# Performance work log

Hardware: AMD Instinct MI355X
Metric: run time of the kernel (lower is better)

## Reference

```python
import jax, jax.numpy as jnp
import numpy as np

N, D, E, H, K = 8192, 1024, 8, 256, 2


def setup_inputs() -> dict:
    key = jax.random.key(0)
    ks = jax.random.split(key, 9)
    s = 0.02
    return {
        "x": jax.random.normal(ks[0], (N, D), dtype=jnp.float32),
        "Wg": jax.random.normal(ks[1], (D, E), dtype=jnp.float32) * s,
        "bg": jnp.zeros((E,), dtype=jnp.float32),
        "W1": jax.random.normal(ks[2], (E, D, H), dtype=jnp.float32) * s,
        "b1": jnp.zeros((E, H), dtype=jnp.float32),
        "W2": jax.random.normal(ks[3], (E, H, H), dtype=jnp.float32) * s,
        "b2": jnp.zeros((E, H), dtype=jnp.float32),
        "W3": jax.random.normal(ks[4], (E, H, D), dtype=jnp.float32) * s,
        "b3": jnp.zeros((E, D), dtype=jnp.float32),
    }


def reference(x, Wg, bg, W1, b1, W2, b2, W3, b3):
    # Gating: softmax over experts, then keep only top-k gate values per token.
    gates = jax.nn.softmax(x @ Wg + bg, axis=-1)              # [N, E]
    top_v, top_i = jax.lax.top_k(gates, K)                    # [N, K]
    rows = jnp.arange(gates.shape[0])[:, None]                # [N, 1]
    top_k_gates = jnp.zeros_like(gates).at[rows, top_i].set(top_v)  # [N, E]

    # Dense all-expert MLP (matches original: every expert runs on every token).
    h = jax.nn.relu(jnp.einsum('nd,edh->neh', x, W1) + b1)    # [N, E, H]
    h = jax.nn.relu(jnp.einsum('neh,ehg->neg', h, W2) + b2)   # [N, E, H]  (dropout is eval no-op)
    eo = jax.nn.relu(jnp.einsum('neh,ehd->ned', h, W3) + b3)  # [N, E, D]

    # Combine with masked gates: einsum('...nde,...ne->...nd') with eo in 'ned' layout.
    output = jnp.einsum('ned,ne->nd', eo, top_k_gates)        # [N, D]
    return output
```

## Files before the change

### kernel.cpp

```cpp
#include <hip/hip_runtime.h>
#include <math.h>

#define NTOK 8192
#define DDIM 1024
#define NEXP 8
#define HDIM 256
#define TOPK 2
#define PADM 128
#define CAPS (NTOK * TOPK + NEXP * PADM)
#define NT64  (CAPS / 64)

typedef __attribute__((ext_vector_type(8))) __bf16 bf16x8;
typedef __attribute__((ext_vector_type(4))) float f32x4;

#define GLDS16(g, s)                                                      \
    __builtin_amdgcn_global_load_lds(                                     \
        (const __attribute__((address_space(1))) void*)(g),               \
        (__attribute__((address_space(3))) void*)(s), 16, 0, 0)

static constexpr size_t OFF_TOFF = 128;
static constexpr size_t OFF_ZBUF = 4096;
static constexpr size_t OFF_T2E  = 8192;
static constexpr size_t OFF_T2G  = OFF_T2E + (size_t)NTOK * TOPK * 4;
static constexpr size_t OFF_SLOT = OFF_T2G + (size_t)NTOK * TOPK * 4;
static constexpr size_t OFF_TOK  = OFF_SLOT + (size_t)NTOK * TOPK * 4;
static constexpr size_t OFF_GAT  = OFF_TOK + (size_t)CAPS * 4;
static constexpr size_t OFF_XB   = (OFF_GAT + (size_t)CAPS * 4 + 255) & ~(size_t)255;
static constexpr size_t OFF_W1T  = OFF_XB  + (size_t)NTOK * DDIM * 2;
static constexpr size_t OFF_W2T  = OFF_W1T + (size_t)NEXP * DDIM * HDIM * 2;
static constexpr size_t OFF_W3T  = OFF_W2T + (size_t)NEXP * HDIM * HDIM * 2;
static constexpr size_t OFF_H2   = OFF_W3T + (size_t)NEXP * HDIM * DDIM * 2;
static constexpr size_t OFF_H3   = OFF_H2  + (size_t)CAPS * HDIM * 2;

static __device__ __forceinline__ unsigned short f2b(float f) {
    __bf16 h = (__bf16)f;
    return __builtin_bit_cast(unsigned short, h);
}
static __device__ __forceinline__ float b2f(unsigned short u) {
    return __builtin_bit_cast(float, ((unsigned)u) << 16);
}

__global__ __launch_bounds__(256) void gate_trans(
    const float* __restrict__ x, const float* __restrict__ Wg,
    const float* __restrict__ bg, unsigned short* __restrict__ xb,
    int* __restrict__ top2e, float* __restrict__ top2g,
    const float* __restrict__ W1, const float* __restrict__ W2,
    const float* __restrict__ W3, __bf16* __restrict__ w1t,
    __bf16* __restrict__ w2t, __bf16* __restrict__ w3t)
{
    __shared__ __align__(16) float sh[NEXP * DDIM];
    const int tid = threadIdx.x;

    if (blockIdx.x < 256) {
        for (int d = tid; d < DDIM; d += 256) {
            const float4 w0 = *(const float4*)(Wg + (size_t)d * NEXP);
            const float4 w1 = *(const float4*)(Wg + (size_t)d * NEXP + 4);
            sh[0 * DDIM + d] = w0.x; sh[1 * DDIM + d] = w0.y;
            sh[2 * DDIM + d] = w0.z; sh[3 * DDIM + d] = w0.w;
            sh[4 * DDIM + d] = w1.x; sh[5 * DDIM + d] = w1.y;
            sh[6 * DDIM + d] = w1.z; sh[7 * DDIM + d] = w1.w;
        }
        __syncthreads();

        const int n = (blockIdx.y * 256 + blockIdx.x) * 4 + (tid >> 6);
        const int lane = tid & 63;
        const float* xr = x + (size_t)n * DDIM;
        unsigned short* xbr = xb + (size_t)n * DDIM;

        float acc[NEXP];
#pragma unroll
        for (int e = 0; e < NEXP; ++e) acc[e] = 0.f;

#pragma unroll
        for (int it = 0; it < 4; ++it) {
            const int d = it * 256 + lane * 4;
            const float4 xv = *(const float4*)(xr + d);
            ushort4 u;
            u.x = f2b(xv.x); u.y = f2b(xv.y); u.z = f2b(xv.z); u.w = f2b(xv.w);
            *(ushort4*)(xbr + d) = u;
#pragma unroll
            for (int e = 0; e < NEXP; ++e) {
                const float4 wt = *(const float4*)(sh + e * DDIM + d);
                acc[e] = fmaf(xv.x, wt.x, acc[e]);
                acc[e] = fmaf(xv.y, wt.y, acc[e]);
                acc[e] = fmaf(xv.z, wt.z, acc[e]);
                acc[e] = fmaf(xv.w, wt.w, acc[e]);
            }
        }
#pragma unroll
        for (int off = 32; off > 0; off >>= 1)
#pragma unroll
            for (int e = 0; e < NEXP; ++e) acc[e] += __shfl_down(acc[e], off, 64);

        if (lane == 0) {
            float v[NEXP], mx = -1e30f;
#pragma unroll
            for (int e = 0; e < NEXP; ++e) { v[e] = acc[e] + bg[e]; mx = fmaxf(mx, v[e]); }
            float p[NEXP], s = 0.f;
#pragma unroll
            for (int e = 0; e < NEXP; ++e) { p[e] = expf(v[e] - mx); s += p[e]; }
            const float inv = 1.f / s;
#pragma unroll
            for (int e = 0; e < NEXP; ++e) p[e] *= inv;
            int i0 = 0;
#pragma unroll
            for (int e = 1; e < NEXP; ++e) if (p[e] > p[i0]) i0 = e;
            int i1 = (i0 == 0) ? 1 : 0;
#pragma unroll
            for (int e = 0; e < NEXP; ++e) if (e != i0 && p[e] > p[i1]) i1 = e;
            top2e[n * 2 + 0] = i0;  top2e[n * 2 + 1] = i1;
            top2g[n * 2 + 0] = p[i0]; top2g[n * 2 + 1] = p[i1];
        }
    } else {
        const int e = blockIdx.y;
        int bt = blockIdx.x - 256;
        const float* Wi; __bf16* Wo; int R, C, xt, yt;
        if (bt < 256)      { Wi = W1; Wo = w1t; R = DDIM; C = HDIM; xt = bt & 7;  yt = bt >> 3; }
        else if (bt < 320) { bt -= 256; Wi = W2; Wo = w2t; R = HDIM; C = HDIM; xt = bt & 7;  yt = bt >> 3; }
        else               { bt -= 320; Wi = W3; Wo = w3t; R = HDIM; C = DDIM; xt = bt & 31; yt = bt >> 5; }
        const int r0 = yt * 32, c0 = xt * 32;
        const int tx = tid & 31, ty = tid >> 5;
        const float* Wie = Wi + (size_t)e * R * C;
        __bf16* Woe = Wo + (size_t)e * C * R;
#pragma unroll
        for (int j = 0; j < 4; ++j)
            sh[(ty + j * 8) * 33 + tx] = Wie[(size_t)(r0 + ty + j * 8) * C + c0 + tx];
        __syncthreads();
#pragma unroll
        for (int j = 0; j < 4; ++j)
            Woe[(size_t)(c0 + ty + j * 8) * R + r0 + tx] = (__bf16)sh[tx * 33 + ty + j * 8];
    }
}

__global__ __launch_bounds__(1024) void route(
    const int* __restrict__ top2e, const float* __restrict__ top2g,
    int* __restrict__ toff, int* __restrict__ tok, float* __restrict__ gat,
    int* __restrict__ slotof, float* __restrict__ zbuf)
{
    const int tid = threadIdx.x;
    const int wv = tid >> 6, ln = tid & 63;
    __shared__ int   waveTot[16][NEXP];
    __shared__ int   waveBase[16][NEXP];
    __shared__ int   totS[NEXP];
    __shared__ int   toffS[NEXP + 1];
    __shared__ short excS[1024][NEXP];

    zbuf[tid] = 0.f;

    int myE[16]; float myG[16];
    const int4*   pe = (const int4*)(top2e + tid * 16);
    const float4* pg = (const float4*)(top2g + tid * 16);
#pragma unroll
    for (int q = 0; q < 4; ++q) {
        const int4 v = pe[q];
        myE[q * 4 + 0] = v.x; myE[q * 4 + 1] = v.y;
        myE[q * 4 + 2] = v.z; myE[q * 4 + 3] = v.w;
        const float4 g = pg[q];
        myG[q * 4 + 0] = g.x; myG[q * 4 + 1] = g.y;
        myG[q * 4 + 2] = g.z; myG[q * 4 + 3] = g.w;
    }

#pragma unroll
    for (int e = 0; e < NEXP; ++e) {
        int c = 0;
#pragma unroll
        for (int j = 0; j < 16; ++j) c += (myE[j] == e);
        int inc = c;
#pragma unroll
        for (int off = 1; off < 64; off <<= 1) {
            const int t = __shfl_up(inc, off, 64);
            if (ln >= off) inc += t;
        }
        excS[tid][e] = (short)(inc - c);
        if (ln == 63) waveTot[wv][e] = inc;
    }
    __syncthreads();

    if (tid < NEXP) {
        int b = 0;
#pragma unroll
        for (int w = 0; w < 16; ++w) {
            const int t = waveTot[w][tid];
            waveBase[w][tid] = b;
            b += t;
        }
        totS[tid] = b;
    }
    __syncthreads();

    if (tid == 0) {
        int acc = 0;
#pragma unroll
        for (int e = 0; e < NEXP; ++e) {
            toffS[e] = acc;
            acc += (totS[e] + PADM - 1) & ~(PADM - 1);
        }
        toffS[NEXP] = acc;
#pragma unroll
        for (int e = 0; e <= NEXP; ++e) toff[e] = toffS[e];
    }
    __syncthreads();

#pragma unroll
    for (int j = 0; j < 16; ++j) {
        int pre = 0;
#pragma unroll
        for (int j2 = 0; j2 < j; ++j2) pre += (myE[j2] == myE[j]);
        const int e = myE[j];
        const int slot = toffS[e] + waveBase[wv][e] + (int)excS[tid][e] + pre;
        const int i = tid * 16 + j;
        tok[slot] = i >> 1;
        gat[slot] = myG[j];
        slotof[i] = slot;
    }

#pragma unroll
    for (int e = 0; e < NEXP; ++e) {
        const int begin = toffS[e] + totS[e];
        const int end   = toffS[e + 1];
        for (int i = begin + tid; i < end; i += 1024) {
            tok[i] = -1;
            gat[i] = 0.f;
        }
    }
}

__global__ __launch_bounds__(256) void egemm123(
    const __bf16* __restrict__ xb, const __bf16* __restrict__ w1t,
    const __bf16* __restrict__ w2t, const __bf16* __restrict__ w3t,
    const float* __restrict__ b1, const float* __restrict__ b2,
    const float* __restrict__ b3, const int* __restrict__ toff,
    const int* __restrict__ tok, const float* __restrict__ gat,
    const char* __restrict__ zbuf, __bf16* __restrict__ h3)
{
    const int total = toff[NEXP];
    const int slot0 = blockIdx.x * 64;
    if (slot0 >= total) return;
    int e = 0;
    while (toff[e + 1] <= slot0) ++e;

    __shared__ __align__(16) char smem[73728];
    char* AsB = smem;
    char* BsB = smem + 8192;
    char* H1s = smem + 40960;

    const int tid  = threadIdx.x;
    const int lane = tid & 63;
    const int wid  = tid >> 6;

    const int srow  = tid >> 3;
    const int sslot = tid & 7;
    const int ks    = sslot ^ (srow & 7);

    const __bf16* We1 = w1t + (size_t)e * HDIM * DDIM;
    const char* ap[2];
#pragma unroll
    for (int i = 0; i < 2; ++i) {
        const int t = tok[slot0 + i * 32 + srow];
        ap[i] = (t >= 0) ? (const char*)(xb + (size_t)t * DDIM + ks * 8)
                         : (const char*)zbuf;
    }
    const char* bp1[8];
#pragma unroll
    for (int i = 0; i < 8; ++i)
        bp1[i] = (const char*)(We1 + (size_t)(i * 32 + srow) * DDIM + ks * 8);

    const int llo = lane & 15, lhi = lane >> 4;
    const int m7 = llo & 7;
    int abyte[4], bbyte[4];
#pragma unroll
    for (int m = 0; m < 4; ++m) {
        abyte[m] = (m * 16 + llo) * 128;
        bbyte[m] = (wid * 64 + m * 16 + llo) * 128;
    }

    f32x4 acc[4][4];
#pragma unroll
    for (int m = 0; m < 4; ++m)
#pragma unroll
        for (int n = 0; n < 4; ++n) acc[m][n] = (f32x4){0.f, 0.f, 0.f, 0.f};

    for (int k0 = 0; k0 < DDIM; k0 += 64) {
        const size_t kb = (size_t)k0 * 2;
        GLDS16(ap[0] + kb, AsB + tid * 16);
        GLDS16(ap[1] + kb, AsB + 4096 + tid * 16);
#pragma unroll
        for (int i = 0; i < 8; ++i)
            GLDS16(bp1[i] + kb, BsB + i * 4096 + tid * 16);
        __syncthreads();
#pragma unroll
        for (int kk = 0; kk < 2; ++kk) {
            const int sl = ((kk << 2) + lhi) ^ m7;
            bf16x8 af[4], bfr[4];
#pragma unroll
            for (int m = 0; m < 4; ++m) af[m]  = *(const bf16x8*)(AsB + abyte[m] + (sl << 4));
#pragma unroll
            for (int n = 0; n < 4; ++n) bfr[n] = *(const bf16x8*)(BsB + bbyte[n] + (sl << 4));
#pragma unroll
            for (int m = 0; m < 4; ++m)
#pragma unroll
                for (int n = 0; n < 4; ++n)
                    acc[m][n] = __builtin_amdgcn_mfma_f32_16x16x32_bf16(
                        af[m], bfr[n], acc[m][n], 0, 0, 0);
        }
        __syncthreads();
    }

    {
        const float* be1 = b1 + (size_t)e * HDIM;
#pragma unroll
        for (int n = 0; n < 4; ++n) {
            const int col = wid * 64 + n * 16 + llo;
            const float bb = be1[col];
            const int colbyte = (col & 7) * 2;
            const int slice = col >> 3;
#pragma unroll
            for (int m = 0; m < 4; ++m) {
#pragma unroll
                for (int j = 0; j < 4; ++j) {
                    const int r = m * 16 + lhi * 4 + j;
                    const float v = fmaxf(acc[m][n][j] + bb, 0.f);
                    *(__bf16*)(H1s + r * 512 + ((slice ^ (r & 7)) << 4) + colbyte) = (__bf16)v;
                }
                acc[m][n] = (f32x4){0.f, 0.f, 0.f, 0.f};
            }
        }
    }
    __syncthreads();

    const __bf16* We2 = w2t + (size_t)e * HDIM * HDIM;
    const char* bp2[8];
#pragma unroll
    for (int i = 0; i < 8; ++i)
        bp2[i] = (const char*)(We2 + (size_t)(i * 32 + srow) * HDIM + ks * 8);

    for (int k2 = 0; k2 < 4; ++k2) {
        const size_t kb = (size_t)k2 * 128;
#pragma unroll
        for (int i = 0; i < 8; ++i)
            GLDS16(bp2[i] + kb, BsB + i * 4096 + tid * 16);
        __syncthreads();
#pragma unroll
        for (int kk = 0; kk < 2; ++kk) {
            const int slB = ((kk << 2) + lhi) ^ m7;
            const int sA  = k2 * 8 + (kk << 2) + lhi;
            const int slA = sA ^ m7;
            bf16x8 af[4], bfr[4];
#pragma unroll
            for (int m = 0; m < 4; ++m)
                af[m] = *(const bf16x8*)(H1s + (m * 16 + llo) * 512 + (slA << 4));
#pragma unroll
            for (int n = 0; n < 4; ++n)
                bfr[n] = *(const bf16x8*)(BsB + bbyte[n] + (slB << 4));
#pragma unroll
            for (int m = 0; m < 4; ++m)
#pragma unroll
                for (int n = 0; n < 4; ++n)
                    acc[m][n] = __builtin_amdgcn_mfma_f32_16x16x32_bf16(
                        af[m], bfr[n], acc[m][n], 0, 0, 0);
        }
        __syncthreads();
    }

    {
        const float* be2 = b2 + (size_t)e * HDIM;
#pragma unroll
        for (int n = 0; n < 4; ++n) {
            const int col = wid * 64 + n * 16 + llo;
            const float bb = be2[col];
            const int colbyte = (col & 7) * 2;
            const int slice = col >> 3;
#pragma unroll
            for (int m = 0; m < 4; ++m) {
#pragma unroll
                for (int j = 0; j < 4; ++j) {
                    const int r = m * 16 + lhi * 4 + j;
                    const float v = fmaxf(acc[m][n][j] + bb, 0.f);
                    *(__bf16*)(H1s + r * 512 + ((slice ^ (r & 7)) << 4) + colbyte) = (__bf16)v;
                }
            }
        }
    }
    __syncthreads();

    const __bf16* We3 = w3t + (size_t)e * DDIM * HDIM;
    const float* be3 = b3 + (size_t)e * DDIM;
    float gv[4][4];
#pragma unroll
    for (int m = 0; m < 4; ++m)
#pragma unroll
        for (int j = 0; j < 4; ++j)
            gv[m][j] = gat[slot0 + m * 16 + lhi * 4 + j];

    for (int cc = 0; cc < 4; ++cc) {
#pragma unroll
        for (int m = 0; m < 4; ++m)
#pragma unroll
            for (int n = 0; n < 4; ++n) acc[m][n] = (f32x4){0.f, 0.f, 0.f, 0.f};

        for (int k2 = 0; k2 < 4; ++k2) {
            const size_t kb = (size_t)k2 * 128;
#pragma unroll
            for (int i = 0; i < 8; ++i)
                GLDS16((const char*)(We3 + (size_t)(cc * 256 + i * 32 + srow) * HDIM + ks * 8) + kb,
                       BsB + i * 4096 + tid * 16);
            __syncthreads();
#pragma unroll
            for (int kk = 0; kk < 2; ++kk) {
                const int slB = ((kk << 2) + lhi) ^ m7;
                const int sA  = k2 * 8 + (kk << 2) + lhi;
                const int slA = sA ^ m7;
                bf16x8 af[4], bfr[4];
#pragma unroll
                for (int m = 0; m < 4; ++m)
                    af[m] = *(const bf16x8*)(H1s + (m * 16 + llo) * 512 + (slA << 4));
#pragma unroll
                for (int n = 0; n < 4; ++n)
                    bfr[n] = *(const bf16x8*)(BsB + bbyte[n] + (slB << 4));
#pragma unroll
                for (int m = 0; m < 4; ++m)
#pragma unroll
                    for (int n = 0; n < 4; ++n)
                        acc[m][n] = __builtin_amdgcn_mfma_f32_16x16x32_bf16(
                            af[m], bfr[n], acc[m][n], 0, 0, 0);
            }
            __syncthreads();
        }

#pragma unroll
        for (int m = 0; m < 4; ++m) {
            const int rbase = slot0 + m * 16 + lhi * 4;
#pragma unroll
            for (int n = 0; n < 4; ++n) {
                const int col = cc * 256 + wid * 64 + n * 16 + llo;
                const float bb = be3[col];
#pragma unroll
                for (int j = 0; j < 4; ++j) {
                    const float v = fmaxf(acc[m][n][j] + bb, 0.f) * gv[m][j];
                    h3[(size_t)(rbase + j) * DDIM + col] = (__bf16)v;
                }
            }
        }
    }
}

__global__ __launch_bounds__(256) void combine(
    const unsigned short* __restrict__ h3, const int* __restrict__ slotof,
    float* __restrict__ out)
{
    const int n = blockIdx.x;
    const int c = threadIdx.x * 4;
    const int s0 = slotof[n * 2], s1 = slotof[n * 2 + 1];
    const ushort4 a = *(const ushort4*)(h3 + (size_t)s0 * DDIM + c);
    const ushort4 b = *(const ushort4*)(h3 + (size_t)s1 * DDIM + c);
    float4 o;
    o.x = b2f(a.x) + b2f(b.x);
    o.y = b2f(a.y) + b2f(b.y);
    o.z = b2f(a.z) + b2f(b.z);
    o.w = b2f(a.w) + b2f(b.w);
    *(float4*)(out + (size_t)n * DDIM + c) = o;
}

extern "C" void kernel_launch(void* const* d_in, const int* in_sizes, int n_in,
                              void* d_out, int out_size, void* d_ws, size_t ws_size,
                              hipStream_t stream)
{
    const float* x  = (const float*)d_in[0];
    const float* Wg = (const float*)d_in[1];
    const float* bg = (const float*)d_in[2];
    const float* W1 = (const float*)d_in[3];
    const float* b1 = (const float*)d_in[4];
    const float* W2 = (const float*)d_in[5];
    const float* b2 = (const float*)d_in[6];
    const float* W3 = (const float*)d_in[7];
    const float* b3 = (const float*)d_in[8];
    float* out = (float*)d_out;

    char* ws = (char*)d_ws;
    int*   toff   = (int*)(ws + OFF_TOFF);
    char*  zbuf   = ws + OFF_ZBUF;
    int*   top2e  = (int*)(ws + OFF_T2E);
    float* top2g  = (float*)(ws + OFF_T2G);
    int*   slotof = (int*)(ws + OFF_SLOT);
    int*   tok    = (int*)(ws + OFF_TOK);
    float* gat    = (float*)(ws + OFF_GAT);
    unsigned short* xbu = (unsigned short*)(ws + OFF_XB);
    __bf16* xb  = (__bf16*)(ws + OFF_XB);
    __bf16* w1t = (__bf16*)(ws + OFF_W1T);
    __bf16* w2t = (__bf16*)(ws + OFF_W2T);
    __bf16* w3t = (__bf16*)(ws + OFF_W3T);
    __bf16* h3  = (__bf16*)(ws + OFF_H3);

    gate_trans<<<dim3(832, NEXP), 256, 0, stream>>>(
        x, Wg, bg, xbu, top2e, top2g, W1, W2, W3, w1t, w2t, w3t);
    route<<<1, 1024, 0, stream>>>(top2e, top2g, toff, tok, gat, slotof, (float*)zbuf);

    egemm123<<<NT64, 256, 0, stream>>>(xb, w1t, w2t, w3t, b1, b2, b3,
                                       toff, tok, gat, zbuf, h3);

    combine<<<NTOK, 256, 0, stream>>>((const unsigned short*)h3, slotof, out);
}
```

Before: 112.0 us.

## Double-buffer LDS tiles across all three expert GEMM stages with cross-stage prefetch

Enlarges shared memory to hold two A/B tile buffers and prefetches the next k-tile with global_load_lds while MFMAs consume the current one. The prefetch also crosses stage boundaries: the first W2 tile is loaded during the last W1 step, and the first W3 tile during the last W2 step. The four W3 column chunks are flattened into one 16-step pipelined loop. The aim is to hide global load latency that the single-buffer load, sync, compute scheme exposed, at the cost of more LDS per block and a possible drop in occupancy.

```diff
diff --git a/kernel.cpp b/kernel.cpp
--- a/kernel.cpp
+++ b/kernel.cpp
@@ -239,10 +239,10 @@
     int e = 0;
     while (toff[e + 1] <= slot0) ++e;
 
-    __shared__ __align__(16) char smem[73728];
-    char* AsB = smem;
-    char* BsB = smem + 8192;
-    char* H1s = smem + 40960;
+    __shared__ __align__(16) char smem[114688];
+    char* As0 = smem;
+    char* Bs0 = smem + 16384;
+    char* H1s = smem + 81920;
 
     const int tid  = threadIdx.x;
     const int lane = tid & 63;
@@ -253,6 +253,8 @@
     const int ks    = sslot ^ (srow & 7);
 
     const __bf16* We1 = w1t + (size_t)e * HDIM * DDIM;
+    const __bf16* We2 = w2t + (size_t)e * HDIM * HDIM;
+    const __bf16* We3 = w3t + (size_t)e * DDIM * HDIM;
     const char* ap[2];
 #pragma unroll
     for (int i = 0; i < 2; ++i) {
@@ -261,9 +263,14 @@
                          : (const char*)zbuf;
     }
     const char* bp1[8];
-#pragma unroll
-    for (int i = 0; i < 8; ++i)
+    const char* bp2[8];
+    const char* bp3[8];
+#pragma unroll
+    for (int i = 0; i < 8; ++i) {
         bp1[i] = (const char*)(We1 + (size_t)(i * 32 + srow) * DDIM + ks * 8);
+        bp2[i] = (const char*)(We2 + (size_t)(i * 32 + srow) * HDIM + ks * 8);
+        bp3[i] = (const char*)(We3 + (size_t)(i * 32 + srow) * HDIM + ks * 8);
+    }
 
     const int llo = lane & 15, lhi = lane >> 4;
     const int m7 = llo & 7;
@@ -274,28 +281,50 @@
         bbyte[m] = (wid * 64 + m * 16 + llo) * 128;
     }
 
+    auto stage1 = [&](int t, int b) {
+        const size_t kb = (size_t)t * 128;
+        GLDS16(ap[0] + kb, As0 + b * 8192 + tid * 16);
+        GLDS16(ap[1] + kb, As0 + b * 8192 + 4096 + tid * 16);
+#pragma unroll
+        for (int i = 0; i < 8; ++i)
+            GLDS16(bp1[i] + kb, Bs0 + b * 32768 + i * 4096 + tid * 16);
+    };
+    auto stage2 = [&](int k2, int b) {
+        const size_t kb = (size_t)k2 * 128;
+#pragma unroll
+        for (int i = 0; i < 8; ++i)
+            GLDS16(bp2[i] + kb, Bs0 + b * 32768 + i * 4096 + tid * 16);
+    };
+    auto stage3 = [&](int idx, int b) {
+        const size_t off = (size_t)(idx >> 2) * 131072 + (size_t)(idx & 3) * 128;
+#pragma unroll
+        for (int i = 0; i < 8; ++i)
+            GLDS16(bp3[i] + off, Bs0 + b * 32768 + i * 4096 + tid * 16);
+    };
+
     f32x4 acc[4][4];
 #pragma unroll
     for (int m = 0; m < 4; ++m)
 #pragma unroll
         for (int n = 0; n < 4; ++n) acc[m][n] = (f32x4){0.f, 0.f, 0.f, 0.f};
 
-    for (int k0 = 0; k0 < DDIM; k0 += 64) {
-        const size_t kb = (size_t)k0 * 2;
-        GLDS16(ap[0] + kb, AsB + tid * 16);
-        GLDS16(ap[1] + kb, AsB + 4096 + tid * 16);
-#pragma unroll
-        for (int i = 0; i < 8; ++i)
-            GLDS16(bp1[i] + kb, BsB + i * 4096 + tid * 16);
-        __syncthreads();
+    stage1(0, 0);
+    __syncthreads();
+
+    for (int t = 0; t < 16; ++t) {
+        const int cb = t & 1, nb = cb ^ 1;
+        if (t < 15) stage1(t + 1, nb);
+        else        stage2(0, nb);
 #pragma unroll
         for (int kk = 0; kk < 2; ++kk) {
             const int sl = ((kk << 2) + lhi) ^ m7;
             bf16x8 af[4], bfr[4];
 #pragma unroll
-            for (int m = 0; m < 4; ++m) af[m]  = *(const bf16x8*)(AsB + abyte[m] + (sl << 4));
-#pragma unroll
-            for (int n = 0; n < 4; ++n) bfr[n] = *(const bf16x8*)(BsB + bbyte[n] + (sl << 4));
+            for (int m = 0; m < 4; ++m)
+                af[m]  = *(const bf16x8*)(As0 + cb * 8192 + abyte[m] + (sl << 4));
+#pragma unroll
+            for (int n = 0; n < 4; ++n)
+                bfr[n] = *(const bf16x8*)(Bs0 + cb * 32768 + bbyte[n] + (sl << 4));
 #pragma unroll
             for (int m = 0; m < 4; ++m)
 #pragma unroll
@@ -328,30 +357,21 @@
     }
     __syncthreads();
 
-    const __bf16* We2 = w2t + (size_t)e * HDIM * HDIM;
-    const char* bp2[8];
-#pragma unroll
-    for (int i = 0; i < 8; ++i)
-        bp2[i] = (const char*)(We2 + (size_t)(i * 32 + srow) * HDIM + ks * 8);
-
     for (int k2 = 0; k2 < 4; ++k2) {
-        const size_t kb = (size_t)k2 * 128;
-#pragma unroll
-        for (int i = 0; i < 8; ++i)
-            GLDS16(bp2[i] + kb, BsB + i * 4096 + tid * 16);
-        __syncthreads();
+        const int cb = k2 & 1, nb = cb ^ 1;
+        if (k2 < 3) stage2(k2 + 1, nb);
+        else        stage3(0, nb);
 #pragma unroll
         for (int kk = 0; kk < 2; ++kk) {
             const int slB = ((kk << 2) + lhi) ^ m7;
-            const int sA  = k2 * 8 + (kk << 2) + lhi;
-            const int slA = sA ^ m7;
+            const int slA = (k2 * 8 + (kk << 2) + lhi) ^ m7;
             bf16x8 af[4], bfr[4];
 #pragma unroll
             for (int m = 0; m < 4; ++m)
                 af[m] = *(const bf16x8*)(H1s + (m * 16 + llo) * 512 + (slA << 4));
 #pragma unroll
             for (int n = 0; n < 4; ++n)
-                bfr[n] = *(const bf16x8*)(BsB + bbyte[n] + (slB << 4));
+                bfr[n] = *(const bf16x8*)(Bs0 + cb * 32768 + bbyte[n] + (slB << 4));
 #pragma unroll
             for (int m = 0; m < 4; ++m)
 #pragma unroll
@@ -378,12 +398,12 @@
                     const float v = fmaxf(acc[m][n][j] + bb, 0.f);
                     *(__bf16*)(H1s + r * 512 + ((slice ^ (r & 7)) << 4) + colbyte) = (__bf16)v;
                 }
+                acc[m][n] = (f32x4){0.f, 0.f, 0.f, 0.f};
             }
         }
     }
     __syncthreads();
 
-    const __bf16* We3 = w3t + (size_t)e * DDIM * HDIM;
     const float* be3 = b3 + (size_t)e * DDIM;
     float gv[4][4];
 #pragma unroll
@@ -392,55 +412,47 @@
         for (int j = 0; j < 4; ++j)
             gv[m][j] = gat[slot0 + m * 16 + lhi * 4 + j];
 
-    for (int cc = 0; cc < 4; ++cc) {
-#pragma unroll
-        for (int m = 0; m < 4; ++m)
-#pragma unroll
-            for (int n = 0; n < 4; ++n) acc[m][n] = (f32x4){0.f, 0.f, 0.f, 0.f};
-
-        for (int k2 = 0; k2 < 4; ++k2) {
-            const size_t kb = (size_t)k2 * 128;
-#pragma unroll
-            for (int i = 0; i < 8; ++i)
-                GLDS16((const char*)(We3 + (size_t)(cc * 256 + i * 32 + srow) * HDIM + ks * 8) + kb,
-                       BsB + i * 4096 + tid * 16);
-            __syncthreads();
-#pragma unroll
-            for (int kk = 0; kk < 2; ++kk) {
-                const int slB = ((kk << 2) + lhi) ^ m7;
-                const int sA  = k2 * 8 + (kk << 2) + lhi;
-                const int slA = sA ^ m7;
-                bf16x8 af[4], bfr[4];
-#pragma unroll
-                for (int m = 0; m < 4; ++m)
-                    af[m] = *(const bf16x8*)(H1s + (m * 16 + llo) * 512 + (slA << 4));
+    for (int idx = 0; idx < 16; ++idx) {
+        const int cb = idx & 1, nb = cb ^ 1;
+        if (idx < 15) stage3(idx + 1, nb);
+        const int k2 = idx & 3;
+#pragma unroll
+        for (int kk = 0; kk < 2; ++kk) {
+            const int slB = ((kk << 2) + lhi) ^ m7;
+            const int slA = (k2 * 8 + (kk << 2) + lhi) ^ m7;
+            bf16x8 af[4], bfr[4];
+#pragma unroll
+            for (int m = 0; m < 4; ++m)
+                af[m] = *(const bf16x8*)(H1s + (m * 16 + llo) * 512 + (slA << 4));
+#pragma unroll
+            for (int n = 0; n < 4; ++n)
+                bfr[n] = *(const bf16x8*)(Bs0 + cb * 32768 + bbyte[n] + (slB << 4));
+#pragma unroll
+            for (int m = 0; m < 4; ++m)
 #pragma unroll
                 for (int n = 0; n < 4; ++n)
-                    bfr[n] = *(const bf16x8*)(BsB + bbyte[n] + (slB << 4));
-#pragma unroll
-                for (int m = 0; m < 4; ++m)
-#pragma unroll
-                    for (int n = 0; n < 4; ++n)
-                        acc[m][n] = __builtin_amdgcn_mfma_f32_16x16x32_bf16(
-                            af[m], bfr[n], acc[m][n], 0, 0, 0);
-            }
-            __syncthreads();
-        }
-
-#pragma unroll
-        for (int m = 0; m < 4; ++m) {
-            const int rbase = slot0 + m * 16 + lhi * 4;
-#pragma unroll
-            for (int n = 0; n < 4; ++n) {
-                const int col = cc * 256 + wid * 64 + n * 16 + llo;
-                const float bb = be3[col];
-#pragma unroll
-                for (int j = 0; j < 4; ++j) {
-                    const float v = fmaxf(acc[m][n][j] + bb, 0.f) * gv[m][j];
-                    h3[(size_t)(rbase + j) * DDIM + col] = (__bf16)v;
+                    acc[m][n] = __builtin_amdgcn_mfma_f32_16x16x32_bf16(
+                        af[m], bfr[n], acc[m][n], 0, 0, 0);
+        }
+        if (k2 == 3) {
+            const int cc = idx >> 2;
+#pragma unroll
+            for (int m = 0; m < 4; ++m) {
+                const int rbase = slot0 + m * 16 + lhi * 4;
+#pragma unroll
+                for (int n = 0; n < 4; ++n) {
+                    const int col = cc * 256 + wid * 64 + n * 16 + llo;
+                    const float bb = be3[col];
+#pragma unroll
+                    for (int j = 0; j < 4; ++j) {
+                        const float v = fmaxf(acc[m][n][j] + bb, 0.f) * gv[m][j];
+                        h3[(size_t)(rbase + j) * DDIM + col] = (__bf16)v;
+                    }
+                    acc[m][n] = (f32x4){0.f, 0.f, 0.f, 0.f};
                 }
             }
         }
+        __syncthreads();
     }
 }
 
```

Result: slower. 127.2 us (+13.5%).
